# Kernel tuning notes

Measured on AMD Instinct MI355X. Metric: run time of the kernel, lower is better.

Reference implementation:

```python
import jax, jax.numpy as jnp
from jax import lax
import numpy as np

MAXDISP = 48
KSIZE = 5
DILATION = 2


def _im2col(z, k, dil):
    # z: [N,1,H,W] -> patches [N, k*k, H, W], same H,W via symmetric padding
    pad = dil * (k - 1) // 2
    return lax.conv_general_dilated_patches(
        z,
        filter_shape=(k, k),
        window_strides=(1, 1),
        padding=[(pad, pad), (pad, pad)],
        rhs_dilation=(dil, dil),
    )


def setup_inputs() -> dict:
    key = jax.random.key(0)
    k1, k2, k3, k4 = jax.random.split(key, 4)
    N, C, H, W = 2, 32, 128, 256
    x = jax.random.normal(k1, (N, C, H, W), dtype=jnp.float32)
    y = jax.random.normal(k2, (N, C, H, W), dtype=jnp.float32)
    filters = jax.random.normal(k3, (N, KSIZE * KSIZE, H, W), dtype=jnp.float32)
    filters_biases = jax.random.normal(k4, (N, 1, H, W), dtype=jnp.float32)
    return {"x": x, "y": y, "filters": filters, "filters_biases": filters_biases}


def reference(x, y, filters, filters_biases):
    N, C, H, W = x.shape
    D = MAXDISP
    # left-pad right feature with D-1 zeros along width
    y_pad = jnp.pad(y, ((0, 0), (0, 0), (0, 0), (D - 1, 0)))
    bias = filters_biases[:, 0]  # [N,H,W]

    def step(carry, start):
        y_sl = lax.dynamic_slice_in_dim(y_pad, start, W, axis=3)  # [N,C,H,W]
        z = jnp.sum(x * y_sl, axis=1, keepdims=True)              # [N,1,H,W]
        p = _im2col(z, KSIZE, DILATION)                            # [N,k*k,H,W]
        out = jnp.sum(p * filters, axis=1) + bias                  # [N,H,W]
        return carry, out

    # disparity i uses slice start D-1-i (torch loop runs d = D-1 .. 0)
    starts = (D - 1) - jnp.arange(D)
    _, corr = lax.scan(step, None, starts)   # [D,N,H,W]
    return jnp.transpose(corr, (1, 0, 2, 3))  # [N,D,H,W]
```

## Files before the change

kernel.cpp:

```cpp
#include <hip/hip_runtime.h>

#define NB 2
#define C 32
#define H 128
#define W 256
#define D 48
#define HW (H * W)

__global__ __launch_bounds__(192) void zkern(const float* __restrict__ x,
                                             const float* __restrict__ y,
                                             float* __restrict__ z) {
    const int s    = blockIdx.x;
    const int xcd  = s & 7;
    const int slot = s >> 3;
    const int half = slot & 1;
    const int t2   = slot >> 1;
    const int hi   = t2 & 15;
    const int n    = t2 >> 4;
    const int h    = xcd * 16 + hi;

    const int tid  = threadIdx.x;
    const int q    = tid & 31;
    const int dg   = tid >> 5;
    const int d0   = dg * 8;

    __shared__ __align__(16) float ys[C][184];

    const float* xrow = x + ((size_t)(n * C) * H + h) * (size_t)W;
    const float* yrow = y + ((size_t)(n * C) * H + h) * (size_t)W;
    const int ybase = 128 * half - 48;

#pragma unroll
    for (int it = 0; it < 8; ++it) {
        const int idx = it * 192 + tid;
        if (idx < 32 * 46) {
            const int r    = idx / 46;
            const int c4   = idx % 46;
            const int yidx = ybase + 4 * c4;
            float4 v = {0.f, 0.f, 0.f, 0.f};
            if (yidx >= 0 && yidx <= W - 4)
                v = *(const float4*)(yrow + (size_t)r * HW + yidx);
            *(float4*)&ys[r][4 * c4] = v;
        }
    }
    __syncthreads();

    float acc[8][4] = {};
    const int S0 = 4 * q + 40 - d0;
    const float* xcol = xrow + 128 * half + 4 * q;

#pragma unroll
    for (int cb = 0; cb < 2; ++cb) {
        float4 xr[16];
#pragma unroll
        for (int t = 0; t < 16; ++t)
            xr[t] = *(const float4*)(xcol + (size_t)(cb * 16 + t) * HW);

#pragma unroll
        for (int t = 0; t < 16; ++t) {
            const int c = cb * 16 + t;
            const float4 w0 = *(const float4*)&ys[c][S0];
            const float4 w1 = *(const float4*)&ys[c][S0 + 4];
            const float4 w2 = *(const float4*)&ys[c][S0 + 8];
            const float win[12] = {w0.x, w0.y, w0.z, w0.w,
                                   w1.x, w1.y, w1.z, w1.w,
                                   w2.x, w2.y, w2.z, w2.w};
            const float xs[4] = {xr[t].x, xr[t].y, xr[t].z, xr[t].w};
#pragma unroll
            for (int k = 0; k < 8; ++k)
#pragma unroll
                for (int o = 0; o < 4; ++o)
                    acc[k][o] += xs[o] * win[8 + o - k];
        }
    }

    float* zp = z + (((size_t)n * D + d0) * H + h) * (size_t)W + 128 * half + 4 * q;
#pragma unroll
    for (int k = 0; k < 8; ++k) {
        float4 v;
        v.x = acc[k][0]; v.y = acc[k][1]; v.z = acc[k][2]; v.w = acc[k][3];
        *(float4*)(zp + (size_t)k * HW) = v;
    }
}

#define DCH 8
#define NCH (D / DCH)

__global__ __launch_bounds__(256) void fkern(const float* __restrict__ z,
                                             const float* __restrict__ Ff,
                                             const float* __restrict__ B,
                                             float* __restrict__ out) {
    __shared__ __align__(16) float zs[DCH][5][264];

    const int s    = blockIdx.x;
    const int xcd  = s & 7;
    const int slot = s >> 3;
    const int ch   = slot % NCH;
    const int t2   = slot / NCH;
    const int hi   = t2 & 15;
    const int n    = t2 >> 4;
    const int h    = xcd * 16 + hi;
    const int d0   = ch * DCH;

    const int tid = threadIdx.x;
    const int q  = tid & 63;
    const int g  = tid >> 6;

#pragma unroll
    for (int it = 0; it < 11; ++it) {
        const int idx = it * 256 + tid;
        if (idx < 40 * 66) {
            const int r  = idx / 66;
            const int c4 = idx % 66;
            const int dd = r / 5;
            const int i  = r % 5;
            const int hh = h + 2 * i - 4;
            float4 v = {0.f, 0.f, 0.f, 0.f};
            if (c4 >= 1 && c4 <= 64 && hh >= 0 && hh < H)
                v = *(const float4*)(z + (((size_t)n * D + d0 + dd) * H + hh) * (size_t)W
                                       + 4 * c4 - 4);
            *(float4*)&zs[dd][i][4 * c4] = v;
        }
    }

    const float4 bias = *(const float4*)(B + ((size_t)n * H + h) * (size_t)W + 4 * q);
    float acc[2][4];
#pragma unroll
    for (int kd = 0; kd < 2; ++kd) {
        acc[kd][0] = bias.x; acc[kd][1] = bias.y;
        acc[kd][2] = bias.z; acc[kd][3] = bias.w;
    }

    __syncthreads();

#pragma unroll
    for (int i = 0; i < 5; ++i) {
        float4 f[5];
#pragma unroll
        for (int jj = 0; jj < 5; ++jj)
            f[jj] = *(const float4*)(Ff + (((size_t)n * 25 + i * 5 + jj) * H + h) * (size_t)W
                                        + 4 * q);
        const float fs[5][4] = {
            {f[0].x, f[0].y, f[0].z, f[0].w},
            {f[1].x, f[1].y, f[1].z, f[1].w},
            {f[2].x, f[2].y, f[2].z, f[2].w},
            {f[3].x, f[3].y, f[3].z, f[3].w},
            {f[4].x, f[4].y, f[4].z, f[4].w}};

#pragma unroll
        for (int kd = 0; kd < 2; ++kd) {
            const int dd = g + 4 * kd;
            const float4 w0 = *(const float4*)&zs[dd][i][4 * q];
            const float4 w1 = *(const float4*)&zs[dd][i][4 * q + 4];
            const float4 w2 = *(const float4*)&zs[dd][i][4 * q + 8];
            const float win[12] = {w0.x, w0.y, w0.z, w0.w,
                                   w1.x, w1.y, w1.z, w1.w,
                                   w2.x, w2.y, w2.z, w2.w};
#pragma unroll
            for (int jj = 0; jj < 5; ++jj)
#pragma unroll
                for (int o = 0; o < 4; ++o)
                    acc[kd][o] += fs[jj][o] * win[o + 2 * jj];
        }
    }

#pragma unroll
    for (int kd = 0; kd < 2; ++kd) {
        float* op = out + (((size_t)n * D + d0 + g + 4 * kd) * H + h) * (size_t)W + 4 * q;
        float4 v;
        v.x = acc[kd][0]; v.y = acc[kd][1]; v.z = acc[kd][2]; v.w = acc[kd][3];
        *(float4*)op = v;
    }
}

__global__ __launch_bounds__(256) void fused_naive(const float* __restrict__ x,
                                                   const float* __restrict__ y,
                                                   const float* __restrict__ Ff,
                                                   const float* __restrict__ B,
                                                   float* __restrict__ out) {
    const size_t idx = (size_t)blockIdx.x * 256 + threadIdx.x;
    if (idx >= (size_t)NB * D * H * W) return;
    const int w = (int)(idx % W);
    const int h = (int)((idx / W) % H);
    const int d = (int)((idx / ((size_t)W * H)) % D);
    const int n = (int)(idx / ((size_t)W * H * D));

    float acc = B[((size_t)n * H + h) * W + w];
#pragma unroll
    for (int i = 0; i < 5; ++i) {
        const int hh = h + 2 * i - 4;
        if (hh < 0 || hh >= H) continue;
#pragma unroll
        for (int j = 0; j < 5; ++j) {
            const int ww = w + 2 * j - 4;
            if (ww < 0 || ww >= W) continue;
            const int ws_ = ww - d;
            float zv = 0.f;
            if (ws_ >= 0) {
                const float* xp = x + (((size_t)n * C) * H + hh) * (size_t)W + ww;
                const float* yp = y + (((size_t)n * C) * H + hh) * (size_t)W + ws_;
                for (int c = 0; c < C; ++c)
                    zv += xp[(size_t)c * HW] * yp[(size_t)c * HW];
            }
            acc += Ff[(((size_t)n * 25 + i * 5 + j) * H + h) * (size_t)W + w] * zv;
        }
    }
    out[idx] = acc;
}

extern "C" void kernel_launch(void* const* d_in, const int* in_sizes, int n_in,
                              void* d_out, int out_size, void* d_ws, size_t ws_size,
                              hipStream_t stream) {
    const float* x = (const float*)d_in[0];
    const float* y = (const float*)d_in[1];
    const float* F = (const float*)d_in[2];
    const float* B = (const float*)d_in[3];
    float* out = (float*)d_out;

    const size_t zbytes = (size_t)NB * D * H * W * sizeof(float);

    if (ws_size >= zbytes) {
        float* z = (float*)d_ws;
        zkern<<<NB * H * 2, 192, 0, stream>>>(x, y, z);
        fkern<<<NB * H * NCH, 256, 0, stream>>>(z, F, B, out);
    } else {
        const size_t total = (size_t)NB * D * H * W;
        fused_naive<<<(int)((total + 255) / 256), 256, 0, stream>>>(x, y, F, B, out);
    }
}
```

Before: 31.85 us.

## Compute two output rows per fkern block to share halo z rows

Each fkern block now produces two output rows (h0 and h0+2) for the same 8 disparities, loading 6 z rows instead of 5 per row, which nearly halves redundant z halo loads. Each thread now accumulates 4 disparities instead of 2, for one row. The grid shrinks to 768 blocks. This lowers global/LDS load traffic but reduces block count and raises per-thread register use.

After: 26.93 us. -15.4%, faster.

```diff
diff --git a/kernel.cpp b/kernel.cpp
--- a/kernel.cpp
+++ b/kernel.cpp
@@ -85,60 +85,65 @@
 
 #define DCH 8
 #define NCH (D / DCH)
+#define FGRID 768
 
 __global__ __launch_bounds__(256) void fkern(const float* __restrict__ z,
                                              const float* __restrict__ Ff,
                                              const float* __restrict__ B,
                                              float* __restrict__ out) {
-    __shared__ __align__(16) float zs[DCH][5][264];
+    __shared__ __align__(16) float zs[DCH][6][264];
 
     const int s    = blockIdx.x;
     const int xcd  = s & 7;
     const int slot = s >> 3;
     const int ch   = slot % NCH;
     const int t2   = slot / NCH;
-    const int hi   = t2 & 15;
-    const int n    = t2 >> 4;
-    const int h    = xcd * 16 + hi;
+    const int p    = t2 & 1;
+    const int pl   = (t2 >> 1) & 3;
+    const int n    = t2 >> 3;
+    const int h0   = xcd * 16 + 4 * pl + p;
     const int d0   = ch * DCH;
 
-    const int tid = threadIdx.x;
-    const int q  = tid & 63;
-    const int g  = tid >> 6;
-
-#pragma unroll
-    for (int it = 0; it < 11; ++it) {
+    const int tid  = threadIdx.x;
+    const int q    = tid & 63;
+    const int r    = (tid >> 6) & 1;
+    const int g2   = tid >> 7;
+    const int hrow = h0 + 2 * r;
+
+#pragma unroll
+    for (int it = 0; it < 13; ++it) {
         const int idx = it * 256 + tid;
-        if (idx < 40 * 66) {
-            const int r  = idx / 66;
+        if (idx < 48 * 66) {
+            const int r2 = idx / 66;
             const int c4 = idx % 66;
-            const int dd = r / 5;
-            const int i  = r % 5;
-            const int hh = h + 2 * i - 4;
+            const int dd = r2 / 6;
+            const int l  = r2 % 6;
+            const int hh = h0 - 4 + 2 * l;
             float4 v = {0.f, 0.f, 0.f, 0.f};
             if (c4 >= 1 && c4 <= 64 && hh >= 0 && hh < H)
                 v = *(const float4*)(z + (((size_t)n * D + d0 + dd) * H + hh) * (size_t)W
                                        + 4 * c4 - 4);
-            *(float4*)&zs[dd][i][4 * c4] = v;
-        }
-    }
-
-    const float4 bias = *(const float4*)(B + ((size_t)n * H + h) * (size_t)W + 4 * q);
-    float acc[2][4];
-#pragma unroll
-    for (int kd = 0; kd < 2; ++kd) {
-        acc[kd][0] = bias.x; acc[kd][1] = bias.y;
-        acc[kd][2] = bias.z; acc[kd][3] = bias.w;
+            *(float4*)&zs[dd][l][4 * c4] = v;
+        }
+    }
+
+    const float4 bias = *(const float4*)(B + ((size_t)n * H + hrow) * (size_t)W + 4 * q);
+    float acc[4][4];
+#pragma unroll
+    for (int k = 0; k < 4; ++k) {
+        acc[k][0] = bias.x; acc[k][1] = bias.y;
+        acc[k][2] = bias.z; acc[k][3] = bias.w;
     }
 
     __syncthreads();
 
 #pragma unroll
     for (int i = 0; i < 5; ++i) {
+        const int l = i + r;
         float4 f[5];
 #pragma unroll
         for (int jj = 0; jj < 5; ++jj)
-            f[jj] = *(const float4*)(Ff + (((size_t)n * 25 + i * 5 + jj) * H + h) * (size_t)W
+            f[jj] = *(const float4*)(Ff + (((size_t)n * 25 + i * 5 + jj) * H + hrow) * (size_t)W
                                         + 4 * q);
         const float fs[5][4] = {
             {f[0].x, f[0].y, f[0].z, f[0].w},
@@ -148,11 +153,11 @@
             {f[4].x, f[4].y, f[4].z, f[4].w}};
 
 #pragma unroll
-        for (int kd = 0; kd < 2; ++kd) {
-            const int dd = g + 4 * kd;
-            const float4 w0 = *(const float4*)&zs[dd][i][4 * q];
-            const float4 w1 = *(const float4*)&zs[dd][i][4 * q + 4];
-            const float4 w2 = *(const float4*)&zs[dd][i][4 * q + 8];
+        for (int k = 0; k < 4; ++k) {
+            const int dd = 4 * g2 + k;
+            const float4 w0 = *(const float4*)&zs[dd][l][4 * q];
+            const float4 w1 = *(const float4*)&zs[dd][l][4 * q + 4];
+            const float4 w2 = *(const float4*)&zs[dd][l][4 * q + 8];
             const float win[12] = {w0.x, w0.y, w0.z, w0.w,
                                    w1.x, w1.y, w1.z, w1.w,
                                    w2.x, w2.y, w2.z, w2.w};
@@ -160,15 +165,15 @@
             for (int jj = 0; jj < 5; ++jj)
 #pragma unroll
                 for (int o = 0; o < 4; ++o)
-                    acc[kd][o] += fs[jj][o] * win[o + 2 * jj];
-        }
-    }
-
-#pragma unroll
-    for (int kd = 0; kd < 2; ++kd) {
-        float* op = out + (((size_t)n * D + d0 + g + 4 * kd) * H + h) * (size_t)W + 4 * q;
+                    acc[k][o] += fs[jj][o] * win[o + 2 * jj];
+        }
+    }
+
+#pragma unroll
+    for (int k = 0; k < 4; ++k) {
+        float* op = out + (((size_t)n * D + d0 + 4 * g2 + k) * H + hrow) * (size_t)W + 4 * q;
         float4 v;
-        v.x = acc[kd][0]; v.y = acc[kd][1]; v.z = acc[kd][2]; v.w = acc[kd][3];
+        v.x = acc[k][0]; v.y = acc[k][1]; v.z = acc[k][2]; v.w = acc[k][3];
         *(float4*)op = v;
     }
 }
@@ -222,7 +227,7 @@
     if (ws_size >= zbytes) {
         float* z = (float*)d_ws;
         zkern<<<NB * H * 2, 192, 0, stream>>>(x, y, z);
-        fkern<<<NB * H * NCH, 256, 0, stream>>>(z, F, B, out);
+        fkern<<<FGRID, 256, 0, stream>>>(z, F, B, out);
     } else {
         const size_t total = (size_t)NB * D * H * W;
         fused_naive<<<(int)((total + 255) / 256), 256, 0, stream>>>(x, y, F, B, out);
```
